# Optimization experiments

Hardware: AMD Instinct MI355X
Metric: run time of the kernel (lower is better)

Reference implementation:

```python
import jax, jax.numpy as jnp
import numpy as np

BETA = 0.25  # args.beta
B, T, D, K = 16, 4096, 64, 1024


def setup_inputs() -> dict:
    key = jax.random.key(0)
    kz, kw = jax.random.split(key)
    z = jax.random.normal(kz, (B, T, D), dtype=jnp.float32)
    # nn.Embedding weight init: uniform(-1/K, 1/K)
    emb = jax.random.uniform(kw, (K, D), dtype=jnp.float32,
                             minval=-1.0 / K, maxval=1.0 / K)
    return {"z": z, "emb": emb}


def reference(z, emb):
    # z: [B, T, D] (torch code loops over first dim; all elements non-empty here)
    # emb: [K, D] codebook
    b, t, d = z.shape
    zf = z.reshape(-1, d)                                   # [B*T, D]
    # squared euclidean distances: ||z||^2 + ||e||^2 - 2 z.e
    dist = (jnp.sum(zf * zf, axis=1, keepdims=True)
            + jnp.sum(emb * emb, axis=1)
            - 2.0 * zf @ emb.T)                             # [B*T, K]
    idx = jnp.argmin(dist, axis=1).reshape(b, t)            # [B, T] int
    z_q_raw = emb[idx]                                      # [B, T, D] gather
    sg = jax.lax.stop_gradient
    # per-batch-element means, summed (loop accumulates loss per z_t)
    commit = jnp.mean((sg(z_q_raw) - z) ** 2, axis=(1, 2))  # [B]
    codebk = jnp.mean((z_q_raw - sg(z)) ** 2, axis=(1, 2))  # [B]
    loss = jnp.sum(BETA * commit + codebk)
    # straight-through estimator
    z_q = z + sg(z_q_raw - z)
    return z_q, loss, idx
```

## Files before the change

### kernel.cpp

```cpp
#include <hip/hip_runtime.h>
#include <math.h>
#include <float.h>

#define NROWS    65536
#define DD       64
#define KK       1024
#define LOSS_OFF 4194304
#define IDX_OFF  4194305
#define RPB      64
#define MAXC     32
#define TPR      4
#define NRND     16

typedef short  short8 __attribute__((ext_vector_type(8)));
typedef float  f32x4  __attribute__((ext_vector_type(4)));

__device__ __forceinline__ void async_copy16(void* lds, const void* g) {
    __builtin_amdgcn_global_load_lds(
        (const __attribute__((address_space(1))) unsigned int*)g,
        (__attribute__((address_space(3))) unsigned int*)lds, 16, 0, 0);
}

__device__ __forceinline__ unsigned short bf16rne(float x) {
    unsigned int u = __float_as_uint(x);
    return (unsigned short)((u + 0x7fffu + ((u >> 16) & 1u)) >> 16);
}

__device__ __forceinline__ float np_sumsq64_stream(const float* p) {
#pragma clang fp contract(off)
    float r[8];
    {
        const float4 u0 = *reinterpret_cast<const float4*>(p);
        const float4 u1 = *reinterpret_cast<const float4*>(p + 4);
        r[0] = u0.x * u0.x; r[1] = u0.y * u0.y; r[2] = u0.z * u0.z; r[3] = u0.w * u0.w;
        r[4] = u1.x * u1.x; r[5] = u1.y * u1.y; r[6] = u1.z * u1.z; r[7] = u1.w * u1.w;
    }
#pragma unroll
    for (int i = 8; i < 64; i += 8) {
        const float4 u0 = *reinterpret_cast<const float4*>(p + i);
        const float4 u1 = *reinterpret_cast<const float4*>(p + i + 4);
        r[0] += u0.x * u0.x; r[1] += u0.y * u0.y; r[2] += u0.z * u0.z; r[3] += u0.w * u0.w;
        r[4] += u1.x * u1.x; r[5] += u1.y * u1.y; r[6] += u1.z * u1.z; r[7] += u1.w * u1.w;
    }
    return ((r[0] + r[1]) + (r[2] + r[3])) + ((r[4] + r[5]) + (r[6] + r[7]));
}

__global__ void vq_prep(const float* __restrict__ emb,
                        float* __restrict__ bn,
                        unsigned short* __restrict__ ebf) {
#pragma clang fp contract(off)
    const int gtid = blockIdx.x * 256 + threadIdx.x;
    const int code = gtid >> 3;
    const int j    = gtid & 7;
    const float* ep = emb + (size_t)code * DD;
    float r = 0.f;
#pragma unroll
    for (int i = 0; i < 8; ++i) {
        const float v = ep[8 * i + j];
        r += v * v;
    }
    const float s1 = r  + __shfl_xor(r,  1, 64);
    const float s2 = s1 + __shfl_xor(s1, 2, 64);
    const float s3 = s2 + __shfl_xor(s2, 4, 64);
    if (j == 0) bn[code] = s3;

    const float* cp = emb + (size_t)gtid * 8;
    const float4 u0 = *reinterpret_cast<const float4*>(cp);
    const float4 u1 = *reinterpret_cast<const float4*>(cp + 4);
    short8 s;
    s[0] = (short)bf16rne(u0.x); s[1] = (short)bf16rne(u0.y);
    s[2] = (short)bf16rne(u0.z); s[3] = (short)bf16rne(u0.w);
    s[4] = (short)bf16rne(u1.x); s[5] = (short)bf16rne(u1.y);
    s[6] = (short)bf16rne(u1.z); s[7] = (short)bf16rne(u1.w);
    *reinterpret_cast<short8*>(ebf + (size_t)gtid * 8) = s;
}

__global__ __launch_bounds__(256)
void vq_main(const float* __restrict__ z, const float* __restrict__ emb,
             const unsigned short* __restrict__ ebf,
             const float* __restrict__ bn, float* __restrict__ out) {
    __shared__ char  dbuf[2][TPR * 2048] __attribute__((aligned(16)));
    __shared__ float a_s[RPB];
    __shared__ float bn_s[KK];
    __shared__ int   cnt[RPB];
    __shared__ int   clist[RPB][MAXC];
    __shared__ int   bidx[RPB];

    const int tid  = threadIdx.x;
    const int lane = tid & 63;
    const int wv   = __builtin_amdgcn_readfirstlane(tid) >> 6;
    const int q    = lane >> 4;
    const int c16  = lane & 15;
    const int rowbase = blockIdx.x * RPB;

    const char* sbase = (const char*)ebf + (size_t)c16 * 128 + (size_t)q * 16;
    char* dst0 = &dbuf[0][wv * 2048 + lane * 16];
    char* dst1 = &dbuf[1][wv * 2048 + lane * 16];

    if (tid < RPB) {
        a_s[tid] = np_sumsq64_stream(z + (size_t)(rowbase + tid) * DD);
        cnt[tid] = 0;
    }
    {
        const int i = tid * 4;
        *reinterpret_cast<float4*>(&bn_s[i]) =
            *reinterpret_cast<const float4*>(bn + i);
    }

    short8 afr[2];
#pragma unroll
    for (int kh = 0; kh < 2; ++kh) {
        const float* zp = z + (size_t)(rowbase + 16 * wv + c16) * DD
                          + 32 * kh + 8 * q;
        const float4 u0 = *reinterpret_cast<const float4*>(zp);
        const float4 u1 = *reinterpret_cast<const float4*>(zp + 4);
        short8 s;
        s[0] = (short)bf16rne(u0.x); s[1] = (short)bf16rne(u0.y);
        s[2] = (short)bf16rne(u0.z); s[3] = (short)bf16rne(u0.w);
        s[4] = (short)bf16rne(u1.x); s[5] = (short)bf16rne(u1.y);
        s[6] = (short)bf16rne(u1.z); s[7] = (short)bf16rne(u1.w);
        afr[kh] = s;
    }

    auto stage = [&](int R, int buf) {
        const char* s0 = sbase + (size_t)(TPR * R + wv) * 2048;
        char* d = buf ? dst1 : dst0;
        async_copy16(d,        s0);
        async_copy16(d + 1024, s0 + 64);
    };

    stage(0, 0);
    __syncthreads();

    float wadd[4];
#pragma unroll
    for (int i = 0; i < 4; ++i) {
        const int rowl = 16 * wv + 4 * q + i;
        wadd[i] = 1.8e-4f * sqrtf(a_s[rowl]) + 1.2e-4f;
    }

    float mn[4];
#pragma unroll
    for (int i = 0; i < 4; ++i) mn[i] = FLT_MAX;

    for (int R = 0; R < NRND; ++R) {
        const int cur = R & 1;
        if (R < NRND - 1) stage(R + 1, cur ^ 1);
        float dv[TPR][4];
#pragma unroll
        for (int j = 0; j < TPR; ++j) {
            const char* tb = &dbuf[cur][j * 2048 + lane * 16];
            const short8 b0 = *reinterpret_cast<const short8*>(tb);
            const short8 b1 = *reinterpret_cast<const short8*>(tb + 1024);
            f32x4 acc = {0.f, 0.f, 0.f, 0.f};
            acc = __builtin_amdgcn_mfma_f32_16x16x32_bf16(afr[0], b0, acc, 0, 0, 0);
            acc = __builtin_amdgcn_mfma_f32_16x16x32_bf16(afr[1], b1, acc, 0, 0, 0);
            const float bnv = bn_s[16 * (TPR * R + j) + c16];
#pragma unroll
            for (int r = 0; r < 4; ++r)
                dv[j][r] = fmaf(-2.f, acc[r], bnv);
        }
#pragma unroll
        for (int j = 0; j < TPR; ++j)
#pragma unroll
            for (int r = 0; r < 4; ++r)
                mn[r] = fminf(mn[r], dv[j][r]);
#pragma unroll
        for (int mask = 1; mask < 16; mask <<= 1)
#pragma unroll
            for (int r = 0; r < 4; ++r)
                mn[r] = fminf(mn[r], __shfl_xor(mn[r], mask, 64));
        float thr[4];
#pragma unroll
        for (int r = 0; r < 4; ++r) thr[r] = mn[r] + wadd[r];
#pragma unroll
        for (int j = 0; j < TPR; ++j) {
            const int col = 16 * (TPR * R + j) + c16;
#pragma unroll
            for (int r = 0; r < 4; ++r) {
                if (dv[j][r] <= thr[r]) {
                    const int rowl = 16 * wv + 4 * q + r;
                    const int slot = atomicAdd(&cnt[rowl], 1);
                    if (slot < MAXC) clist[rowl][slot] = col;
                }
            }
        }
        __syncthreads();
    }

    {
        const int rowl = 16 * wv + c16;
        const int row  = rowbase + rowl;
        const int nc   = cnt[rowl];
        const bool full = nc > MAXC;
        const int lim  = full ? KK : nc;
        const float av = a_s[rowl];
        const float* zp = z + (size_t)row * DD;
        float sb = FLT_MAX;
        int   cb = 0x7fffffff;
        for (int jj = q; jj < lim; jj += 4) {
            const int c = full ? jj : clist[rowl][jj];
            const float* ep = emb + (size_t)c * DD;
            float dot = 0.f;
#pragma unroll
            for (int d = 0; d < DD; d += 4) {
                const float4 zv = *reinterpret_cast<const float4*>(zp + d);
                const float4 ev = *reinterpret_cast<const float4*>(ep + d);
                dot = fmaf(zv.x, ev.x, dot); dot = fmaf(zv.y, ev.y, dot);
                dot = fmaf(zv.z, ev.z, dot); dot = fmaf(zv.w, ev.w, dot);
            }
            const float tt = av + bn_s[c];
            const float sd = fmaf(-2.f, dot, tt);
            if (sd < sb || (sd == sb && c < cb)) { sb = sd; cb = c; }
        }
#pragma unroll
        for (int mask = 16; mask < 64; mask <<= 1) {
            const float so = __shfl_xor(sb, mask, 64);
            const int   co = __shfl_xor(cb, mask, 64);
            if (so < sb || (so == sb && co < cb)) { sb = so; cb = co; }
        }
        if (cb > 1023) cb = 0;
        if (q == 0) bidx[rowl] = cb;
    }
    __syncthreads();

    if (tid >= RPB) return;
    const int row = rowbase + tid;
    const int bid = bidx[tid];
    const float* ep = emb + (size_t)bid * DD;
    const float* zp = z + (size_t)row * DD;
    float* op = out + (size_t)row * DD;
    double sac = 0.0;
#pragma unroll
    for (int d = 0; d < DD; d += 4) {
        const float4 zv = *reinterpret_cast<const float4*>(zp + d);
        const float4 e4 = *reinterpret_cast<const float4*>(ep + d);
        const float df0 = e4.x - zv.x;
        const float df1 = e4.y - zv.y;
        const float df2 = e4.z - zv.z;
        const float df3 = e4.w - zv.w;
        float4 qv;
        qv.x = zv.x + df0; qv.y = zv.y + df1;
        qv.z = zv.z + df2; qv.w = zv.w + df3;
        *reinterpret_cast<float4*>(op + d) = qv;
        sac += (double)(df0 * df0); sac += (double)(df1 * df1);
        sac += (double)(df2 * df2); sac += (double)(df3 * df3);
    }
    out[IDX_OFF + row] = (float)bid;

#pragma unroll
    for (int off = 32; off > 0; off >>= 1) sac += __shfl_down(sac, off, 64);
    if (lane == 0)
        atomicAdd(&out[LOSS_OFF], (float)((1.25 * sac) / 262144.0));
}

extern "C" void kernel_launch(void* const* d_in, const int* in_sizes, int n_in,
                              void* d_out, int out_size, void* d_ws, size_t ws_size,
                              hipStream_t stream) {
    const float* z   = (const float*)d_in[0];
    const float* emb = (const float*)d_in[1];
    float* out = (float*)d_out;

    float*          bnw = (float*)d_ws;
    unsigned short* ebf = (unsigned short*)((char*)d_ws + 4096);

    vq_prep<<<dim3(32), dim3(256), 0, stream>>>(emb, bnw, ebf);
    vq_main<<<dim3(NROWS / RPB), dim3(256), 0, stream>>>(z, emb, ebf, bnw, out);
}
```

Before: 124.2 us.

## Halve rows per block and split codebook columns across wave pairs

Each block now handles 32 rows instead of 64. The four waves are arranged as two row tiles times two codebook halves, so each wave processes one 16-column tile per round over 32 rounds. The refinement step splits candidates across both column-half waves and merges their results through shared memory. The goal is more blocks and finer-grained work per wave to improve occupancy and latency hiding, at the cost of twice as many rounds and __syncthreads calls per block, more redundant bn/staging setup, and a smaller candidate list (MAXC 24).

New measurement: 279.0 us. 2.25x slower.

```diff
diff --git a/kernel.cpp b/kernel.cpp
--- a/kernel.cpp
+++ b/kernel.cpp
@@ -7,10 +7,9 @@
 #define KK       1024
 #define LOSS_OFF 4194304
 #define IDX_OFF  4194305
-#define RPB      64
-#define MAXC     32
-#define TPR      4
-#define NRND     16
+#define RPB      32
+#define MAXC     24
+#define NRND     32
 
 typedef short  short8 __attribute__((ext_vector_type(8)));
 typedef float  f32x4  __attribute__((ext_vector_type(4)));
@@ -79,23 +78,26 @@
 void vq_main(const float* __restrict__ z, const float* __restrict__ emb,
              const unsigned short* __restrict__ ebf,
              const float* __restrict__ bn, float* __restrict__ out) {
-    __shared__ char  dbuf[2][TPR * 2048] __attribute__((aligned(16)));
+    __shared__ char  dbuf[2][2][2048] __attribute__((aligned(16)));
     __shared__ float a_s[RPB];
     __shared__ float bn_s[KK];
     __shared__ int   cnt[RPB];
     __shared__ int   clist[RPB][MAXC];
     __shared__ int   bidx[RPB];
+    __shared__ float sred_s[RPB][2];
+    __shared__ int   sred_c[RPB][2];
 
     const int tid  = threadIdx.x;
     const int lane = tid & 63;
     const int wv   = __builtin_amdgcn_readfirstlane(tid) >> 6;
+    const int rt   = wv >> 1;
+    const int ch   = wv & 1;
     const int q    = lane >> 4;
     const int c16  = lane & 15;
     const int rowbase = blockIdx.x * RPB;
 
-    const char* sbase = (const char*)ebf + (size_t)c16 * 128 + (size_t)q * 16;
-    char* dst0 = &dbuf[0][wv * 2048 + lane * 16];
-    char* dst1 = &dbuf[1][wv * 2048 + lane * 16];
+    const char* sbase = (const char*)ebf + (size_t)c16 * 128
+                        + (size_t)rt * 64 + (size_t)q * 16;
 
     if (tid < RPB) {
         a_s[tid] = np_sumsq64_stream(z + (size_t)(rowbase + tid) * DD);
@@ -110,7 +112,7 @@
     short8 afr[2];
 #pragma unroll
     for (int kh = 0; kh < 2; ++kh) {
-        const float* zp = z + (size_t)(rowbase + 16 * wv + c16) * DD
+        const float* zp = z + (size_t)(rowbase + 16 * rt + c16) * DD
                           + 32 * kh + 8 * q;
         const float4 u0 = *reinterpret_cast<const float4*>(zp);
         const float4 u1 = *reinterpret_cast<const float4*>(zp + 4);
@@ -123,10 +125,9 @@
     }
 
     auto stage = [&](int R, int buf) {
-        const char* s0 = sbase + (size_t)(TPR * R + wv) * 2048;
-        char* d = buf ? dst1 : dst0;
-        async_copy16(d,        s0);
-        async_copy16(d + 1024, s0 + 64);
+        const char* s0 = sbase + (size_t)(32 * ch + R) * 2048;
+        char* d = &dbuf[buf][ch][rt * 1024 + lane * 16];
+        async_copy16(d, s0);
     };
 
     stage(0, 0);
@@ -135,7 +136,7 @@
     float wadd[4];
 #pragma unroll
     for (int i = 0; i < 4; ++i) {
-        const int rowl = 16 * wv + 4 * q + i;
+        const int rowl = 16 * rt + 4 * q + i;
         wadd[i] = 1.8e-4f * sqrtf(a_s[rowl]) + 1.2e-4f;
     }
 
@@ -146,59 +147,49 @@
     for (int R = 0; R < NRND; ++R) {
         const int cur = R & 1;
         if (R < NRND - 1) stage(R + 1, cur ^ 1);
-        float dv[TPR][4];
-#pragma unroll
-        for (int j = 0; j < TPR; ++j) {
-            const char* tb = &dbuf[cur][j * 2048 + lane * 16];
-            const short8 b0 = *reinterpret_cast<const short8*>(tb);
-            const short8 b1 = *reinterpret_cast<const short8*>(tb + 1024);
-            f32x4 acc = {0.f, 0.f, 0.f, 0.f};
-            acc = __builtin_amdgcn_mfma_f32_16x16x32_bf16(afr[0], b0, acc, 0, 0, 0);
-            acc = __builtin_amdgcn_mfma_f32_16x16x32_bf16(afr[1], b1, acc, 0, 0, 0);
-            const float bnv = bn_s[16 * (TPR * R + j) + c16];
-#pragma unroll
-            for (int r = 0; r < 4; ++r)
-                dv[j][r] = fmaf(-2.f, acc[r], bnv);
-        }
-#pragma unroll
-        for (int j = 0; j < TPR; ++j)
-#pragma unroll
-            for (int r = 0; r < 4; ++r)
-                mn[r] = fminf(mn[r], dv[j][r]);
+        const int g = 32 * ch + R;
+        const char* tb = &dbuf[cur][ch][lane * 16];
+        const short8 b0 = *reinterpret_cast<const short8*>(tb);
+        const short8 b1 = *reinterpret_cast<const short8*>(tb + 1024);
+        f32x4 acc = {0.f, 0.f, 0.f, 0.f};
+        acc = __builtin_amdgcn_mfma_f32_16x16x32_bf16(afr[0], b0, acc, 0, 0, 0);
+        acc = __builtin_amdgcn_mfma_f32_16x16x32_bf16(afr[1], b1, acc, 0, 0, 0);
+        const float bnv = bn_s[16 * g + c16];
+        float dv[4];
+#pragma unroll
+        for (int r = 0; r < 4; ++r) {
+            dv[r] = fmaf(-2.f, acc[r], bnv);
+            mn[r] = fminf(mn[r], dv[r]);
+        }
 #pragma unroll
         for (int mask = 1; mask < 16; mask <<= 1)
 #pragma unroll
             for (int r = 0; r < 4; ++r)
                 mn[r] = fminf(mn[r], __shfl_xor(mn[r], mask, 64));
-        float thr[4];
-#pragma unroll
-        for (int r = 0; r < 4; ++r) thr[r] = mn[r] + wadd[r];
-#pragma unroll
-        for (int j = 0; j < TPR; ++j) {
-            const int col = 16 * (TPR * R + j) + c16;
-#pragma unroll
-            for (int r = 0; r < 4; ++r) {
-                if (dv[j][r] <= thr[r]) {
-                    const int rowl = 16 * wv + 4 * q + r;
-                    const int slot = atomicAdd(&cnt[rowl], 1);
-                    if (slot < MAXC) clist[rowl][slot] = col;
-                }
+        const int col = 16 * g + c16;
+#pragma unroll
+        for (int r = 0; r < 4; ++r) {
+            if (dv[r] <= mn[r] + wadd[r]) {
+                const int rowl = 16 * rt + 4 * q + r;
+                const int slot = atomicAdd(&cnt[rowl], 1);
+                if (slot < MAXC) clist[rowl][slot] = col;
             }
         }
         __syncthreads();
     }
 
     {
-        const int rowl = 16 * wv + c16;
+        const int rowl = 16 * rt + c16;
         const int row  = rowbase + rowl;
         const int nc   = cnt[rowl];
         const bool full = nc > MAXC;
         const int lim  = full ? KK : nc;
+        const int sub  = 2 * q + ch;
         const float av = a_s[rowl];
         const float* zp = z + (size_t)row * DD;
         float sb = FLT_MAX;
         int   cb = 0x7fffffff;
-        for (int jj = q; jj < lim; jj += 4) {
+        for (int jj = sub; jj < lim; jj += 8) {
             const int c = full ? jj : clist[rowl][jj];
             const float* ep = emb + (size_t)c * DD;
             float dot = 0.f;
@@ -219,8 +210,15 @@
             const int   co = __shfl_xor(cb, mask, 64);
             if (so < sb || (so == sb && co < cb)) { sb = so; cb = co; }
         }
+        if (lane < 16) { sred_s[rowl][ch] = sb; sred_c[rowl][ch] = cb; }
+    }
+    __syncthreads();
+    if (tid < RPB) {
+        const float s0 = sred_s[tid][0], s1 = sred_s[tid][1];
+        const int   c0 = sred_c[tid][0], c1 = sred_c[tid][1];
+        int cb = (s1 < s0 || (s1 == s0 && c1 < c0)) ? c1 : c0;
         if (cb > 1023) cb = 0;
-        if (q == 0) bidx[rowl] = cb;
+        bidx[tid] = cb;
     }
     __syncthreads();
 
@@ -249,8 +247,8 @@
     out[IDX_OFF + row] = (float)bid;
 
 #pragma unroll
-    for (int off = 32; off > 0; off >>= 1) sac += __shfl_down(sac, off, 64);
-    if (lane == 0)
+    for (int off = 16; off > 0; off >>= 1) sac += __shfl_down(sac, off, 64);
+    if (tid == 0)
         atomicAdd(&out[LOSS_OFF], (float)((1.25 * sac) / 262144.0));
 }
 
```
